# Performance work log

Measured on AMD Instinct MI355X. Metric: run time of the kernel, lower is better.

## Reference

```python
import jax, jax.numpy as jnp
import numpy as np

IN_C = 128
HID = 128
LEAF = 50000
N0, W = 100000, 16
N1, N2 = 25000, 5000
E1, E2 = 500000, 100000


def setup_inputs() -> dict:
    key = jax.random.key(0)
    ks = jax.random.split(key, 16)
    emb = jax.random.normal(ks[0], (LEAF, IN_C), jnp.float32) * 0.02
    emb = emb.at[0].set(0.0)  # padding_idx=0
    inp = {
        "x": jax.random.randint(ks[1], (N0, W), 0, LEAF),
        "src1": jax.random.randint(ks[2], (E1,), 0, N0),
        "dst1": jax.random.randint(ks[3], (E1,), 0, N1),
        "src2": jax.random.randint(ks[4], (E2,), 0, N1),
        "dst2": jax.random.randint(ks[5], (E2,), 0, N2),
        "n1": N1,
        "n2": N2,
        "emb": emb,
        "ln_g": jnp.ones((IN_C,), jnp.float32),
        "ln_b": jnp.zeros((IN_C,), jnp.float32),
        "Wl1": jax.random.normal(ks[6], (HID, IN_C), jnp.float32) * 0.05,
        "bl1": jnp.zeros((HID,), jnp.float32),
        "Wr1": jax.random.normal(ks[7], (HID, IN_C), jnp.float32) * 0.05,
        "Wl2": jax.random.normal(ks[8], (HID, HID), jnp.float32) * 0.05,
        "bl2": jnp.zeros((HID,), jnp.float32),
        "Wr2": jax.random.normal(ks[9], (HID, HID), jnp.float32) * 0.05,
    }
    return inp


def _layernorm(h, g, b, eps=1e-5):
    mu = jnp.mean(h, axis=-1, keepdims=True)
    var = jnp.mean(jnp.square(h - mu), axis=-1, keepdims=True)
    return (h - mu) * jax.lax.rsqrt(var + eps) * g + b


def _sage_conv(h, src, dst, n_tgt, Wl, bl, Wr):
    # bipartite SAGEConv with mean aggregation (PyG default):
    # out = lin_l(mean_j h[src_j -> i]) + lin_r(h[:n_tgt])
    msg = h[src]  # [E, C] irregular gather
    agg = jax.ops.segment_sum(msg, dst, num_segments=n_tgt)
    cnt = jax.ops.segment_sum(jnp.ones((src.shape[0],), h.dtype), dst, num_segments=n_tgt)
    mean = agg / jnp.maximum(cnt, 1.0)[:, None]
    return mean @ Wl.T + bl + h[:n_tgt] @ Wr.T


def reference(x, src1, dst1, src2, dst2, n1, n2, emb, ln_g, ln_b,
              Wl1, bl1, Wr1, Wl2, bl2, Wr2):
    h = jnp.sum(emb[x], axis=1)               # [N0, C] embedding-bag sum
    h = jax.nn.relu(_layernorm(h, ln_g, ln_b))
    h = _sage_conv(h, src1, dst1, n1, Wl1, bl1, Wr1)
    h = jax.nn.relu(h)                        # dropout: eval mode -> identity
    h = _sage_conv(h, src2, dst2, n2, Wl2, bl2, Wr2)
    return h
```

## Files before the change

kernel.cpp:

```cpp
#include <hip/hip_runtime.h>

#define C 128
#define LDSPAD 136
#define CAP 64

typedef unsigned int uint;
typedef unsigned short ushort;
typedef __attribute__((ext_vector_type(8))) short bf16x8;
typedef __attribute__((ext_vector_type(4))) float f32x4;
typedef __attribute__((ext_vector_type(4))) float nf4;

__device__ __forceinline__ float bf_lo(uint u) { return __uint_as_float(u << 16); }
__device__ __forceinline__ float bf_hi(uint u) { return __uint_as_float(u & 0xffff0000u); }
__device__ __forceinline__ uint f2bf(float f) {
  uint u = __float_as_uint(f);
  return (u + 0x7fffu + ((u >> 16) & 1u)) >> 16;
}
__device__ __forceinline__ uint pk2(float a, float b) {
  return f2bf(a) | (f2bf(b) << 16);
}

__global__ __launch_bounds__(256) void k_prep(
    const float* __restrict__ emb, ushort4* __restrict__ embh, int n4,
    const float4* __restrict__ w0, const float4* __restrict__ w1,
    const float4* __restrict__ w2, const float4* __restrict__ w3,
    ushort4* __restrict__ wb, int nw4each,
    int4* __restrict__ zb, int nz4) {
  int i = blockIdx.x * blockDim.x + threadIdx.x;
  if (i < n4) {
    nf4 f = __builtin_nontemporal_load((const nf4*)emb + i);
    ushort4 o = {(ushort)f2bf(f.x), (ushort)f2bf(f.y), (ushort)f2bf(f.z), (ushort)f2bf(f.w)};
    embh[i] = o;
  }
  if (i < 4 * nw4each) {
    int m = i / nw4each;
    int j = i - m * nw4each;
    const float4* w = (m == 0) ? w0 : (m == 1) ? w1 : (m == 2) ? w2 : w3;
    float4 f = w[j];
    ushort4 o = {(ushort)f2bf(f.x), (ushort)f2bf(f.y), (ushort)f2bf(f.z), (ushort)f2bf(f.w)};
    wb[i] = o;
  }
  if (i < nz4) {
    int4 z = {0, 0, 0, 0};
    zb[i] = z;
  }
}

__device__ __forceinline__ void ln_relu_store(const float s[8], float4 ga, float4 gb,
                                              float4 ba, float4 bb, ushort* hrow,
                                              int c, bool store) {
  float loc = ((s[0] + s[1]) + (s[2] + s[3])) + ((s[4] + s[5]) + (s[6] + s[7]));
#pragma unroll
  for (int off = 8; off; off >>= 1) loc += __shfl_xor(loc, off, 64);
  float mu = loc * (1.f / C);
  float d[8];
  float sq = 0.f;
#pragma unroll
  for (int j = 0; j < 8; ++j) {
    d[j] = s[j] - mu;
    sq += d[j] * d[j];
  }
#pragma unroll
  for (int off = 8; off; off >>= 1) sq += __shfl_xor(sq, off, 64);
  float rs = rsqrtf(sq * (1.f / C) + 1e-5f);
  float o0 = fmaxf(d[0] * rs * ga.x + ba.x, 0.f);
  float o1 = fmaxf(d[1] * rs * ga.y + ba.y, 0.f);
  float o2 = fmaxf(d[2] * rs * ga.z + ba.z, 0.f);
  float o3 = fmaxf(d[3] * rs * ga.w + ba.w, 0.f);
  float o4 = fmaxf(d[4] * rs * gb.x + bb.x, 0.f);
  float o5 = fmaxf(d[5] * rs * gb.y + bb.y, 0.f);
  float o6 = fmaxf(d[6] * rs * gb.z + bb.z, 0.f);
  float o7 = fmaxf(d[7] * rs * gb.w + bb.w, 0.f);
  uint4 o = {pk2(o0, o1), pk2(o2, o3), pk2(o4, o5), pk2(o6, o7)};
  if (store) *(uint4*)(hrow + c * 8) = o;
}

__global__ __launch_bounds__(256) void k_embed_bkt(
    const int* __restrict__ x, const ushort* __restrict__ emb,
    const float* __restrict__ g, const float* __restrict__ b,
    ushort* __restrict__ h, int n0,
    const int* __restrict__ src1, const int* __restrict__ dst1,
    int* __restrict__ cnt1, int* __restrict__ slots1, int e1,
    const int* __restrict__ src2, const int* __restrict__ dst2,
    int* __restrict__ cnt2, int* __restrict__ slots2, int e2,
    int bktBlocks, int totBlocks) {
  uint bid = blockIdx.x;
  uint f0 = (bid * (uint)bktBlocks) / (uint)totBlocks;
  uint f1 = ((bid + 1u) * (uint)bktBlocks) / (uint)totBlocks;
  if (f1 > f0) {
    int i = (int)f0 * 256 + (int)threadIdx.x;
    if (i < e1) {
      int d = __builtin_nontemporal_load(&dst1[i]);
      int s = __builtin_nontemporal_load(&src1[i]);
      int p = atomicAdd(&cnt1[d], 1);
      if (p < CAP) __builtin_nontemporal_store(s, &slots1[d * CAP + p]);
    } else if (i < e1 + e2) {
      int j = i - e1;
      int d = __builtin_nontemporal_load(&dst2[j]);
      int s = __builtin_nontemporal_load(&src2[j]);
      int p = atomicAdd(&cnt2[d], 1);
      if (p < CAP) __builtin_nontemporal_store(s, &slots2[d * CAP + p]);
    }
    return;
  }
  int eb = (int)(bid - f0);
  int wid = threadIdx.x >> 6;
  int lane = threadIdx.x & 63;
  int grp = lane >> 4;
  int c = lane & 15;
  int node0 = (eb * 4 + wid) * 4;
  if (node0 >= n0) return;
  int xv0 = __builtin_nontemporal_load(&x[(size_t)(node0 + 0) * 16 + c]);
  int xv1 = __builtin_nontemporal_load(&x[(size_t)(node0 + 1) * 16 + c]);
  int xv2 = __builtin_nontemporal_load(&x[(size_t)(node0 + 2) * 16 + c]);
  int xv3 = __builtin_nontemporal_load(&x[(size_t)(node0 + 3) * 16 + c]);
  float s[4][8];
#pragma unroll
  for (int n = 0; n < 4; ++n)
#pragma unroll
    for (int j = 0; j < 8; ++j) s[n][j] = 0.f;
#pragma unroll
  for (int w = 0; w < 4; ++w) {
    int t0 = __shfl(xv0, w * 4 + grp, 64);
    int t1 = __shfl(xv1, w * 4 + grp, 64);
    int t2 = __shfl(xv2, w * 4 + grp, 64);
    int t3 = __shfl(xv3, w * 4 + grp, 64);
    uint4 u0 = ((const uint4*)(emb + (size_t)t0 * C))[c];
    uint4 u1 = ((const uint4*)(emb + (size_t)t1 * C))[c];
    uint4 u2 = ((const uint4*)(emb + (size_t)t2 * C))[c];
    uint4 u3 = ((const uint4*)(emb + (size_t)t3 * C))[c];
    s[0][0] += bf_lo(u0.x); s[0][1] += bf_hi(u0.x);
    s[0][2] += bf_lo(u0.y); s[0][3] += bf_hi(u0.y);
    s[0][4] += bf_lo(u0.z); s[0][5] += bf_hi(u0.z);
    s[0][6] += bf_lo(u0.w); s[0][7] += bf_hi(u0.w);
    s[1][0] += bf_lo(u1.x); s[1][1] += bf_hi(u1.x);
    s[1][2] += bf_lo(u1.y); s[1][3] += bf_hi(u1.y);
    s[1][4] += bf_lo(u1.z); s[1][5] += bf_hi(u1.z);
    s[1][6] += bf_lo(u1.w); s[1][7] += bf_hi(u1.w);
    s[2][0] += bf_lo(u2.x); s[2][1] += bf_hi(u2.x);
    s[2][2] += bf_lo(u2.y); s[2][3] += bf_hi(u2.y);
    s[2][4] += bf_lo(u2.z); s[2][5] += bf_hi(u2.z);
    s[2][6] += bf_lo(u2.w); s[2][7] += bf_hi(u2.w);
    s[3][0] += bf_lo(u3.x); s[3][1] += bf_hi(u3.x);
    s[3][2] += bf_lo(u3.y); s[3][3] += bf_hi(u3.y);
    s[3][4] += bf_lo(u3.z); s[3][5] += bf_hi(u3.z);
    s[3][6] += bf_lo(u3.w); s[3][7] += bf_hi(u3.w);
  }
#pragma unroll
  for (int n = 0; n < 4; ++n)
#pragma unroll
    for (int j = 0; j < 8; ++j) {
      s[n][j] += __shfl_xor(s[n][j], 16, 64);
      s[n][j] += __shfl_xor(s[n][j], 32, 64);
    }
  float4 ga = ((const float4*)g)[c * 2];
  float4 gb = ((const float4*)g)[c * 2 + 1];
  float4 ba = ((const float4*)b)[c * 2];
  float4 bb = ((const float4*)b)[c * 2 + 1];
#pragma unroll
  for (int n = 0; n < 4; ++n)
    ln_relu_store(s[n], ga, gb, ba, bb, h + (size_t)(node0 + n) * C, c, grp == 0);
}

template <bool RELU, bool BF16OUT>
__global__ __launch_bounds__(512) void k_conv(
    const int* __restrict__ cntArr, const int* __restrict__ slots,
    const ushort* __restrict__ h, const ushort* __restrict__ Wlb,
    const float* __restrict__ bl, const ushort* __restrict__ Wrb,
    void* __restrict__ outp, int ntgt) {
  __shared__ __align__(16) ushort smean[16 * LDSPAD];
  int wave = threadIdx.x >> 6;
  int lane = threadIdx.x & 63;
  int grp = lane >> 5, sub = lane & 31;
  int mbase = blockIdx.x * 16;
  int nl = wave * 2 + grp;
  int node = mbase + nl;

  int truecnt = (node < ntgt) ? cntArr[node] : 0;
  int cnt = min(truecnt, CAP);
  const int* sl = slots + (size_t)(node < ntgt ? node : 0) * CAP;
  int ev = (sub < cnt) ? sl[sub] : 0;
  int ev2 = (sub + 32 < cnt) ? sl[sub + 32] : 0;
  int dmax = max(cnt, __shfl_xor(cnt, 32, 64));
  int half = grp * 32;
  int l16 = (lane >> 4) & 1;
  int c = lane & 15;
  float s[8];
#pragma unroll
  for (int j = 0; j < 8; ++j) s[j] = 0.f;
  for (int d = 0; d < dmax; d += 8) {
#pragma unroll
    for (int k = 0; k < 4; ++k) {
      int p = d + 2 * k + l16;
      int e = (p < 32) ? __shfl(ev, half + p, 64) : __shfl(ev2, half + p - 32, 64);
      uint4 u = ((const uint4*)(h + (size_t)e * C))[c];
      uint msk = (p < cnt) ? 0xffffffffu : 0u;
      u.x &= msk; u.y &= msk; u.z &= msk; u.w &= msk;
      s[0] += bf_lo(u.x); s[1] += bf_hi(u.x);
      s[2] += bf_lo(u.y); s[3] += bf_hi(u.y);
      s[4] += bf_lo(u.z); s[5] += bf_hi(u.z);
      s[6] += bf_lo(u.w); s[7] += bf_hi(u.w);
    }
  }
#pragma unroll
  for (int j = 0; j < 8; ++j) s[j] += __shfl_xor(s[j], 16, 64);
  float sc = 1.f / (float)max(truecnt, 1);
  uint4 o = {pk2(s[0] * sc, s[1] * sc), pk2(s[2] * sc, s[3] * sc),
             pk2(s[4] * sc, s[5] * sc), pk2(s[6] * sc, s[7] * sc)};
  if (l16 == 0) *(uint4*)(smean + nl * LDSPAD + c * 8) = o;
  __syncthreads();

  int r16 = lane & 15;
  int quad = lane >> 4;
  int koff = quad * 8;
  bf16x8 am[4], ah[4];
  int hr = min(mbase + r16, ntgt - 1);
  const ushort* hrow = h + (size_t)hr * C;
#pragma unroll
  for (int kc = 0; kc < 4; ++kc) {
    am[kc] = *(const bf16x8*)(smean + r16 * LDSPAD + kc * 32 + koff);
    ah[kc] = *(const bf16x8*)(hrow + kc * 32 + koff);
  }
  int nbase = wave * 16;
  float bias = bl[nbase + r16];
  f32x4 acc = {bias, bias, bias, bias};
  const ushort* wlrow = Wlb + (size_t)(nbase + r16) * C;
  const ushort* wrrow = Wrb + (size_t)(nbase + r16) * C;
#pragma unroll
  for (int kc = 0; kc < 4; ++kc) {
    bf16x8 wl = *(const bf16x8*)(wlrow + kc * 32 + koff);
    acc = __builtin_amdgcn_mfma_f32_16x16x32_bf16(am[kc], wl, acc, 0, 0, 0);
    bf16x8 wr = *(const bf16x8*)(wrrow + kc * 32 + koff);
    acc = __builtin_amdgcn_mfma_f32_16x16x32_bf16(ah[kc], wr, acc, 0, 0, 0);
  }
#pragma unroll
  for (int r = 0; r < 4; ++r) {
    int row = mbase + quad * 4 + r;
    if (row < ntgt) {
      float v = acc[r];
      if (RELU) v = fmaxf(v, 0.f);
      if (BF16OUT)
        ((ushort*)outp)[(size_t)row * C + nbase + r16] = (ushort)f2bf(v);
      else
        ((float*)outp)[(size_t)row * C + nbase + r16] = v;
    }
  }
}

extern "C" void kernel_launch(void* const* d_in, const int* in_sizes, int n_in,
                              void* d_out, int out_size, void* d_ws, size_t ws_size,
                              hipStream_t stream) {
  const int*   x    = (const int*)d_in[0];
  const int*   src1 = (const int*)d_in[1];
  const int*   dst1 = (const int*)d_in[2];
  const int*   src2 = (const int*)d_in[3];
  const int*   dst2 = (const int*)d_in[4];
  const float* emb  = (const float*)d_in[7];
  const float* ln_g = (const float*)d_in[8];
  const float* ln_b = (const float*)d_in[9];
  const float* Wl1  = (const float*)d_in[10];
  const float* bl1  = (const float*)d_in[11];
  const float* Wr1  = (const float*)d_in[12];
  const float* Wl2  = (const float*)d_in[13];
  const float* bl2  = (const float*)d_in[14];
  const float* Wr2  = (const float*)d_in[15];

  const int N0 = in_sizes[0] / 16;
  const int E1 = in_sizes[1];
  const int E2 = in_sizes[3];
  const int N1 = 25000;
  const int N2 = 5000;
  const int LEAF_ELEMS = in_sizes[7];
  const int W_ELEMS = C * C;

  char* ws = (char*)d_ws;
  size_t off = 0;
  auto alloc = [&](size_t bytes) {
    char* p = ws + off;
    off += (bytes + 255) & ~(size_t)255;
    return p;
  };
  ushort* embh   = (ushort*)alloc((size_t)LEAF_ELEMS * 2);
  ushort* h0     = (ushort*)alloc((size_t)N0 * C * 2);
  ushort* h1     = (ushort*)alloc((size_t)N1 * C * 2);
  ushort* wb     = (ushort*)alloc((size_t)4 * W_ELEMS * 2);
  int*    slots1 = (int*)alloc((size_t)N1 * CAP * 4);
  int*    slots2 = (int*)alloc((size_t)N2 * CAP * 4);
  char*   zbase  = ws + off;
  int*    cnt1   = (int*)alloc((size_t)N1 * 4);
  int*    cnt2   = (int*)alloc((size_t)N2 * 4);
  size_t  zbytes = (size_t)((ws + off) - zbase);

  float* out = (float*)d_out;
  ushort* Wl1b = wb;
  ushort* Wr1b = wb + W_ELEMS;
  ushort* Wl2b = wb + 2 * W_ELEMS;
  ushort* Wr2b = wb + 3 * W_ELEMS;

  {
    int n4 = LEAF_ELEMS / 4;
    int nw4each = W_ELEMS / 4;
    int nz4 = (int)(zbytes / 16);
    k_prep<<<(n4 + 255) / 256, 256, 0, stream>>>(
        emb, (ushort4*)embh, n4,
        (const float4*)Wl1, (const float4*)Wr1, (const float4*)Wl2, (const float4*)Wr2,
        (ushort4*)wb, nw4each, (int4*)zbase, nz4);
  }

  {
    int bktBlocks = (E1 + E2 + 255) / 256;
    int embBlocks = (N0 + 15) / 16;
    int totBlocks = bktBlocks + embBlocks;
    k_embed_bkt<<<totBlocks, 256, 0, stream>>>(
        x, embh, ln_g, ln_b, h0, N0,
        src1, dst1, cnt1, slots1, E1,
        src2, dst2, cnt2, slots2, E2, bktBlocks, totBlocks);
  }

  k_conv<true, true><<<(N1 + 15) / 16, 512, 0, stream>>>(
      cnt1, slots1, h0, Wl1b, bl1, Wr1b, h1, N1);

  k_conv<false, false><<<(N2 + 15) / 16, 512, 0, stream>>>(
      cnt2, slots2, h1, Wl2b, bl2, Wr2b, out, N2);
}
```

Measured before the change: 216.3 us.

## Fold edge bucketing into embedding waves to overlap atomics with gather latency

```diff
diff --git a/kernel.cpp b/kernel.cpp
--- a/kernel.cpp
+++ b/kernel.cpp
@@ -75,40 +75,27 @@
   if (store) *(uint4*)(hrow + c * 8) = o;
 }
 
-__global__ __launch_bounds__(256) void k_embed_bkt(
+__device__ __forceinline__ void acc8(float s[8], uint4 u) {
+  s[0] += bf_lo(u.x); s[1] += bf_hi(u.x);
+  s[2] += bf_lo(u.y); s[3] += bf_hi(u.y);
+  s[4] += bf_lo(u.z); s[5] += bf_hi(u.z);
+  s[6] += bf_lo(u.w); s[7] += bf_hi(u.w);
+}
+
+__global__ __launch_bounds__(256) void k_embed_fused(
     const int* __restrict__ x, const ushort* __restrict__ emb,
     const float* __restrict__ g, const float* __restrict__ b,
     ushort* __restrict__ h, int n0,
     const int* __restrict__ src1, const int* __restrict__ dst1,
     int* __restrict__ cnt1, int* __restrict__ slots1, int e1,
     const int* __restrict__ src2, const int* __restrict__ dst2,
-    int* __restrict__ cnt2, int* __restrict__ slots2, int e2,
-    int bktBlocks, int totBlocks) {
-  uint bid = blockIdx.x;
-  uint f0 = (bid * (uint)bktBlocks) / (uint)totBlocks;
-  uint f1 = ((bid + 1u) * (uint)bktBlocks) / (uint)totBlocks;
-  if (f1 > f0) {
-    int i = (int)f0 * 256 + (int)threadIdx.x;
-    if (i < e1) {
-      int d = __builtin_nontemporal_load(&dst1[i]);
-      int s = __builtin_nontemporal_load(&src1[i]);
-      int p = atomicAdd(&cnt1[d], 1);
-      if (p < CAP) __builtin_nontemporal_store(s, &slots1[d * CAP + p]);
-    } else if (i < e1 + e2) {
-      int j = i - e1;
-      int d = __builtin_nontemporal_load(&dst2[j]);
-      int s = __builtin_nontemporal_load(&src2[j]);
-      int p = atomicAdd(&cnt2[d], 1);
-      if (p < CAP) __builtin_nontemporal_store(s, &slots2[d * CAP + p]);
-    }
-    return;
-  }
-  int eb = (int)(bid - f0);
+    int* __restrict__ cnt2, int* __restrict__ slots2, int e2) {
   int wid = threadIdx.x >> 6;
   int lane = threadIdx.x & 63;
   int grp = lane >> 4;
   int c = lane & 15;
-  int node0 = (eb * 4 + wid) * 4;
+  int gw = blockIdx.x * 4 + wid;
+  int node0 = gw * 4;
   if (node0 >= n0) return;
   int xv0 = __builtin_nontemporal_load(&x[(size_t)(node0 + 0) * 16 + c]);
   int xv1 = __builtin_nontemporal_load(&x[(size_t)(node0 + 1) * 16 + c]);
@@ -119,8 +106,42 @@
   for (int n = 0; n < 4; ++n)
 #pragma unroll
     for (int j = 0; j < 8; ++j) s[n][j] = 0.f;
-#pragma unroll
-  for (int w = 0; w < 4; ++w) {
+
+  uint4 ua[2][4];
+#pragma unroll
+  for (int w = 0; w < 2; ++w) {
+    int t0 = __shfl(xv0, w * 4 + grp, 64);
+    int t1 = __shfl(xv1, w * 4 + grp, 64);
+    int t2 = __shfl(xv2, w * 4 + grp, 64);
+    int t3 = __shfl(xv3, w * 4 + grp, 64);
+    ua[w][0] = ((const uint4*)(emb + (size_t)t0 * C))[c];
+    ua[w][1] = ((const uint4*)(emb + (size_t)t1 * C))[c];
+    ua[w][2] = ((const uint4*)(emb + (size_t)t2 * C))[c];
+    ua[w][3] = ((const uint4*)(emb + (size_t)t3 * C))[c];
+  }
+
+  if (lane < 24) {
+    int i = gw * 24 + lane;
+    if (i < e1) {
+      int d = __builtin_nontemporal_load(&dst1[i]);
+      int sv = __builtin_nontemporal_load(&src1[i]);
+      int p = atomicAdd(&cnt1[d], 1);
+      if (p < CAP) __builtin_nontemporal_store(sv, &slots1[d * CAP + p]);
+    } else {
+      int j = i - e1;
+      int d = __builtin_nontemporal_load(&dst2[j]);
+      int sv = __builtin_nontemporal_load(&src2[j]);
+      int p = atomicAdd(&cnt2[d], 1);
+      if (p < CAP) __builtin_nontemporal_store(sv, &slots2[d * CAP + p]);
+    }
+  }
+
+#pragma unroll
+  for (int w = 0; w < 2; ++w)
+#pragma unroll
+    for (int n = 0; n < 4; ++n) acc8(s[n], ua[w][n]);
+#pragma unroll
+  for (int w = 2; w < 4; ++w) {
     int t0 = __shfl(xv0, w * 4 + grp, 64);
     int t1 = __shfl(xv1, w * 4 + grp, 64);
     int t2 = __shfl(xv2, w * 4 + grp, 64);
@@ -129,23 +150,9 @@
     uint4 u1 = ((const uint4*)(emb + (size_t)t1 * C))[c];
     uint4 u2 = ((const uint4*)(emb + (size_t)t2 * C))[c];
     uint4 u3 = ((const uint4*)(emb + (size_t)t3 * C))[c];
-    s[0][0] += bf_lo(u0.x); s[0][1] += bf_hi(u0.x);
-    s[0][2] += bf_lo(u0.y); s[0][3] += bf_hi(u0.y);
-    s[0][4] += bf_lo(u0.z); s[0][5] += bf_hi(u0.z);
-    s[0][6] += bf_lo(u0.w); s[0][7] += bf_hi(u0.w);
-    s[1][0] += bf_lo(u1.x); s[1][1] += bf_hi(u1.x);
-    s[1][2] += bf_lo(u1.y); s[1][3] += bf_hi(u1.y);
-    s[1][4] += bf_lo(u1.z); s[1][5] += bf_hi(u1.z);
-    s[1][6] += bf_lo(u1.w); s[1][7] += bf_hi(u1.w);
-    s[2][0] += bf_lo(u2.x); s[2][1] += bf_hi(u2.x);
-    s[2][2] += bf_lo(u2.y); s[2][3] += bf_hi(u2.y);
-    s[2][4] += bf_lo(u2.z); s[2][5] += bf_hi(u2.z);
-    s[2][6] += bf_lo(u2.w); s[2][7] += bf_hi(u2.w);
-    s[3][0] += bf_lo(u3.x); s[3][1] += bf_hi(u3.x);
-    s[3][2] += bf_lo(u3.y); s[3][3] += bf_hi(u3.y);
-    s[3][4] += bf_lo(u3.z); s[3][5] += bf_hi(u3.z);
-    s[3][6] += bf_lo(u3.w); s[3][7] += bf_hi(u3.w);
-  }
+    acc8(s[0], u0); acc8(s[1], u1); acc8(s[2], u2); acc8(s[3], u3);
+  }
+
 #pragma unroll
   for (int n = 0; n < 4; ++n)
 #pragma unroll
@@ -308,13 +315,11 @@
   }
 
   {
-    int bktBlocks = (E1 + E2 + 255) / 256;
     int embBlocks = (N0 + 15) / 16;
-    int totBlocks = bktBlocks + embBlocks;
-    k_embed_bkt<<<totBlocks, 256, 0, stream>>>(
+    k_embed_fused<<<embBlocks, 256, 0, stream>>>(
         x, embh, ln_g, ln_b, h0, N0,
         src1, dst1, cnt1, slots1, E1,
-        src2, dst2, cnt2, slots2, E2, bktBlocks, totBlocks);
+        src2, dst2, cnt2, slots2, E2);
   }
 
   k_conv<true, true><<<(N1 + 15) / 16, 512, 0, stream>>>(
```

Result: no change. 220.4 us (+1.9%).

## Fold edge bucketing into every embed wave and spread LayerNorm across lane groups

Applied to the files above, without the earlier changes.

```diff
diff --git a/kernel.cpp b/kernel.cpp
--- a/kernel.cpp
+++ b/kernel.cpp
@@ -47,8 +47,7 @@
 }
 
 __device__ __forceinline__ void ln_relu_store(const float s[8], float4 ga, float4 gb,
-                                              float4 ba, float4 bb, ushort* hrow,
-                                              int c, bool store) {
+                                              float4 ba, float4 bb, ushort* hrow, int c) {
   float loc = ((s[0] + s[1]) + (s[2] + s[3])) + ((s[4] + s[5]) + (s[6] + s[7]));
 #pragma unroll
   for (int off = 8; off; off >>= 1) loc += __shfl_xor(loc, off, 64);
@@ -72,10 +71,10 @@
   float o6 = fmaxf(d[6] * rs * gb.z + bb.z, 0.f);
   float o7 = fmaxf(d[7] * rs * gb.w + bb.w, 0.f);
   uint4 o = {pk2(o0, o1), pk2(o2, o3), pk2(o4, o5), pk2(o6, o7)};
-  if (store) *(uint4*)(hrow + c * 8) = o;
-}
-
-__global__ __launch_bounds__(256) void k_embed_bkt(
+  *(uint4*)(hrow + c * 8) = o;
+}
+
+__global__ __launch_bounds__(256) void k_embed_sf(
     const int* __restrict__ x, const ushort* __restrict__ emb,
     const float* __restrict__ g, const float* __restrict__ b,
     ushort* __restrict__ h, int n0,
@@ -83,37 +82,36 @@
     int* __restrict__ cnt1, int* __restrict__ slots1, int e1,
     const int* __restrict__ src2, const int* __restrict__ dst2,
     int* __restrict__ cnt2, int* __restrict__ slots2, int e2,
-    int bktBlocks, int totBlocks) {
-  uint bid = blockIdx.x;
-  uint f0 = (bid * (uint)bktBlocks) / (uint)totBlocks;
-  uint f1 = ((bid + 1u) * (uint)bktBlocks) / (uint)totBlocks;
-  if (f1 > f0) {
-    int i = (int)f0 * 256 + (int)threadIdx.x;
-    if (i < e1) {
-      int d = __builtin_nontemporal_load(&dst1[i]);
-      int s = __builtin_nontemporal_load(&src1[i]);
-      int p = atomicAdd(&cnt1[d], 1);
-      if (p < CAP) __builtin_nontemporal_store(s, &slots1[d * CAP + p]);
-    } else if (i < e1 + e2) {
-      int j = i - e1;
-      int d = __builtin_nontemporal_load(&dst2[j]);
-      int s = __builtin_nontemporal_load(&src2[j]);
-      int p = atomicAdd(&cnt2[d], 1);
-      if (p < CAP) __builtin_nontemporal_store(s, &slots2[d * CAP + p]);
-    }
-    return;
-  }
-  int eb = (int)(bid - f0);
+    int epw) {
   int wid = threadIdx.x >> 6;
   int lane = threadIdx.x & 63;
   int grp = lane >> 4;
   int c = lane & 15;
-  int node0 = (eb * 4 + wid) * 4;
+  int gw = blockIdx.x * 4 + wid;
+  int node0 = gw * 4;
   if (node0 >= n0) return;
+
   int xv0 = __builtin_nontemporal_load(&x[(size_t)(node0 + 0) * 16 + c]);
   int xv1 = __builtin_nontemporal_load(&x[(size_t)(node0 + 1) * 16 + c]);
   int xv2 = __builtin_nontemporal_load(&x[(size_t)(node0 + 2) * 16 + c]);
   int xv3 = __builtin_nontemporal_load(&x[(size_t)(node0 + 3) * 16 + c]);
+
+  for (int t = lane; t < epw; t += 64) {
+    int i = gw * epw + t;
+    if (i < e1) {
+      int d = __builtin_nontemporal_load(&dst1[i]);
+      int sv = __builtin_nontemporal_load(&src1[i]);
+      int p = atomicAdd(&cnt1[d], 1);
+      if (p < CAP) __builtin_nontemporal_store(sv, &slots1[d * CAP + p]);
+    } else if (i < e1 + e2) {
+      int j = i - e1;
+      int d = __builtin_nontemporal_load(&dst2[j]);
+      int sv = __builtin_nontemporal_load(&src2[j]);
+      int p = atomicAdd(&cnt2[d], 1);
+      if (p < CAP) __builtin_nontemporal_store(sv, &slots2[d * CAP + p]);
+    }
+  }
+
   float s[4][8];
 #pragma unroll
   for (int n = 0; n < 4; ++n)
@@ -153,13 +151,15 @@
       s[n][j] += __shfl_xor(s[n][j], 16, 64);
       s[n][j] += __shfl_xor(s[n][j], 32, 64);
     }
+  float sel[8];
+#pragma unroll
+  for (int j = 0; j < 8; ++j)
+    sel[j] = (grp == 0) ? s[0][j] : (grp == 1) ? s[1][j] : (grp == 2) ? s[2][j] : s[3][j];
   float4 ga = ((const float4*)g)[c * 2];
   float4 gb = ((const float4*)g)[c * 2 + 1];
   float4 ba = ((const float4*)b)[c * 2];
   float4 bb = ((const float4*)b)[c * 2 + 1];
-#pragma unroll
-  for (int n = 0; n < 4; ++n)
-    ln_relu_store(s[n], ga, gb, ba, bb, h + (size_t)(node0 + n) * C, c, grp == 0);
+  ln_relu_store(sel, ga, gb, ba, bb, h + (size_t)(node0 + grp) * C, c);
 }
 
 template <bool RELU, bool BF16OUT>
@@ -308,13 +308,13 @@
   }
 
   {
-    int bktBlocks = (E1 + E2 + 255) / 256;
     int embBlocks = (N0 + 15) / 16;
-    int totBlocks = bktBlocks + embBlocks;
-    k_embed_bkt<<<totBlocks, 256, 0, stream>>>(
+    int nwaves = embBlocks * 4;
+    int epw = (E1 + E2 + nwaves - 1) / nwaves;
+    k_embed_sf<<<embBlocks, 256, 0, stream>>>(
         x, embh, ln_g, ln_b, h0, N0,
         src1, dst1, cnt1, slots1, E1,
-        src2, dst2, cnt2, slots2, E2, bktBlocks, totBlocks);
+        src2, dst2, cnt2, slots2, E2, epw);
   }
 
   k_conv<true, true><<<(N1 + 15) / 16, 512, 0, stream>>>(
```

Measured after the change: 221.1 us. +2.2%, slower.
